# Performance work log

Measured on AMD Instinct MI355X. Metric: run time of the kernel, lower is better.

Reference implementation:

```python
import jax, jax.numpy as jnp
import numpy as np

MAX_DEPTH = 9
HIDDEN = 64
EMB = 64
POS_FREQS = 6
IN_C = 1
SIZES = [4 ** d for d in range(MAX_DEPTH + 1)]
OFFSETS = np.concatenate([[0], np.cumsum(SIZES)])  # per-depth slices into concatenated node arrays
TOTAL = int(OFFSETS[-1])  # 349525
POS_DIM = 3 + 2 * POS_FREQS * 3  # 39


def _interleave(v):
    v = v & 0xFFFF
    v = (v | (v << 8)) & 0x00FF00FF
    v = (v | (v << 4)) & 0x0F0F0F0F
    v = (v | (v << 2)) & 0x33333333
    v = (v | (v << 1)) & 0x55555555
    return v


def _deinterleave(v):
    v = v & 0x55555555
    v = (v | (v >> 1)) & 0x33333333
    v = (v | (v >> 2)) & 0x0F0F0F0F
    v = (v | (v >> 4)) & 0x00FF00FF
    v = (v | (v >> 8)) & 0x0000FFFF
    return v


def _xy(d):
    keys = jnp.arange(4 ** d, dtype=jnp.int32)  # full tree: sorted Morton keys = arange
    return _deinterleave(keys), _deinterleave(keys >> 1)


def _neighbors(d):
    # [N, 9] neighbor indices in Morton order grid; -1 outside the image (matches quadtree.neighs padding)
    ix, iy = _xy(d)
    res = 1 << d
    cols = []
    for dy in (-1, 0, 1):
        for dx in (-1, 0, 1):
            nx, ny = ix + dx, iy + dy
            valid = (nx >= 0) & (nx < res) & (ny >= 0) & (ny < res)
            key = _interleave(nx) | (_interleave(ny) << 1)
            cols.append(jnp.where(valid, key, -1))
    return jnp.stack(cols, axis=1)


def _pos_enc(d):
    # node_centers_from_keys + fourier_encode
    ix, iy = _xy(d)
    res = float(1 << d)
    x = (ix.astype(jnp.float32) + 0.5) / res
    y = (iy.astype(jnp.float32) + 0.5) / res
    dn = jnp.full_like(x, float(d) / float(MAX_DEPTH))
    pos = jnp.stack([x, y, dn], axis=1)  # [N, 3]
    freqs = 2.0 ** jnp.arange(POS_FREQS, dtype=jnp.float32)
    ang = pos[:, :, None] * (2.0 * np.pi) * freqs  # [N, 3, F]
    enc = jnp.concatenate([jnp.sin(ang), jnp.cos(ang)], axis=-1).reshape(pos.shape[0], -1)  # [N, 3*2F]
    return jnp.concatenate([pos, enc], axis=1)  # [N, 39]


def setup_inputs() -> dict:
    key = jax.random.key(0)
    ks = jax.random.split(key, 10)
    s = 0.05
    return {
        "features_in": jax.random.normal(ks[0], (TOTAL, IN_C), jnp.float32),
        "in_proj_W": jax.random.normal(ks[1], (IN_C + POS_DIM, HIDDEN), jnp.float32) * s,
        "in_proj_b": jnp.zeros((HIDDEN,), jnp.float32),
        "conv_W": jax.random.normal(ks[2], (MAX_DEPTH + 1, 9 * HIDDEN, HIDDEN), jnp.float32) * s,
        "conv_b": jnp.zeros((MAX_DEPTH + 1, HIDDEN), jnp.float32),
        "emb_W": jax.random.normal(ks[3], (MAX_DEPTH + 1, HIDDEN, EMB), jnp.float32) * s,
        "emb_b": jnp.zeros((MAX_DEPTH + 1, EMB), jnp.float32),
        "ln_g": jnp.ones((MAX_DEPTH + 1, EMB), jnp.float32),
        "ln_b": jnp.zeros((MAX_DEPTH + 1, EMB), jnp.float32),
        "depth_gain": jnp.ones((MAX_DEPTH + 1,), jnp.float32),
    }


def reference(features_in, in_proj_W, in_proj_b, conv_W, conv_b, emb_W, emb_b, ln_g, ln_b, depth_gain):
    D = MAX_DEPTH
    # per-depth input projection with fourier positional encoding
    h = []
    for d in range(D + 1):
        f = features_in[OFFSETS[d]:OFFSETS[d + 1]]
        x = jnp.concatenate([f, _pos_enc(d)], axis=1)  # [N_d, in_c + 39]
        h.append(x @ in_proj_W + in_proj_b)
    # bottom-up: QuadPool (mean over 4 children; full tree => children of parent i are 4i..4i+3) + QuadConv
    for d in range(D, 0, -1):
        Np = 4 ** (d - 1)
        pooled = h[d].reshape(Np, 4, HIDDEN).mean(axis=1)
        hd1 = h[d - 1] + pooled
        if d - 1 >= 1:
            neigh = _neighbors(d - 1)  # [N, 9], -1 at borders
            N = neigh.shape[0]
            padded = jnp.concatenate([hd1, jnp.zeros((1, HIDDEN), hd1.dtype)], axis=0)
            gi = jnp.where(neigh < 0, N, neigh)
            col = padded[gi].reshape(N, 9 * HIDDEN)
            hd1 = jax.nn.relu(col @ conv_W[d - 1] + conv_b[d - 1])
        h[d - 1] = hd1
    # per-depth embedding head: Linear -> LayerNorm -> depth gain
    outs = []
    eps = 1e-5
    for d in range(D + 1):
        z = h[d] @ emb_W[d] + emb_b[d]
        mu = z.mean(-1, keepdims=True)
        var = ((z - mu) ** 2).mean(-1, keepdims=True)
        z = (z - mu) / jnp.sqrt(var + eps) * ln_g[d] + ln_b[d]
        outs.append(depth_gain[d] * z)
    return jnp.concatenate(outs, axis=0)  # [TOTAL, EMB] (E[0]..E[max_depth] concatenated)
```

## Files before the change

### kernel.cpp

```cpp
#include <hip/hip_runtime.h>
#include <hip/hip_bf16.h>

static constexpr int TOTAL = 349525;
static constexpr int OFFS[11] = {0,1,5,21,85,341,1365,5461,21845,87381,349525};
static constexpr size_t CONV_USH = (size_t)8*9*2*4*64*8;
static constexpr size_t EMB_USH  = (size_t)10*2*4*64*8;
static constexpr size_t FRAG_USH = CONV_USH + EMB_USH;
static constexpr size_t FRAG_BYTES = FRAG_USH*2*2;
static constexpr size_t HPRE_BYTES = (size_t)(87381-85)*64*4;

typedef __attribute__((ext_vector_type(8))) short short8;
typedef __attribute__((ext_vector_type(4))) float f32x4;

__device__ __forceinline__ unsigned deint(unsigned v){
  v &= 0x55555555u;
  v = (v | (v>>1)) & 0x33333333u;
  v = (v | (v>>2)) & 0x0F0F0F0Fu;
  v = (v | (v>>4)) & 0x00FF00FFu;
  v = (v | (v>>8)) & 0x0000FFFFu;
  return v;
}
__device__ __forceinline__ unsigned ileave(unsigned v){
  v &= 0xFFFFu;
  v = (v | (v<<8)) & 0x00FF00FFu;
  v = (v | (v<<4)) & 0x0F0F0F0Fu;
  v = (v | (v<<2)) & 0x33333333u;
  v = (v | (v<<1)) & 0x55555555u;
  return v;
}
__device__ __forceinline__ unsigned short f2bh(float x){
  unsigned u = __float_as_uint(x);
  return (unsigned short)((u + 0x7FFFu + ((u>>16)&1u)) >> 16);
}
__device__ __forceinline__ float bh2f(unsigned short h){
  return __uint_as_float(((unsigned)h) << 16);
}
__device__ __forceinline__ void split8(float4 a, float4 b, short8 &hi, short8 &lo){
  float v[8] = {a.x,a.y,a.z,a.w,b.x,b.y,b.z,b.w};
  unsigned short hv[8], lv[8];
  #pragma unroll
  for (int j=0;j<8;++j){ hv[j]=f2bh(v[j]); lv[j]=f2bh(v[j]-bh2f(hv[j])); }
  hi = short8{(short)hv[0],(short)hv[1],(short)hv[2],(short)hv[3],
              (short)hv[4],(short)hv[5],(short)hv[6],(short)hv[7]};
  lo = short8{(short)lv[0],(short)lv[1],(short)lv[2],(short)lv[3],
              (short)lv[4],(short)lv[5],(short)lv[6],(short)lv[7]};
}

__global__ __launch_bounds__(256) void k_wprep(const float* __restrict__ convW,
    const float* __restrict__ embW,
    unsigned short* __restrict__ WH, unsigned short* __restrict__ WLo){
  int tid = blockIdx.x*256 + threadIdx.x;
  if (tid >= 41984) return;
  const float* src;
  size_t dst;
  if (tid < 36864){
    int l=tid&63, cb=(tid>>6)&3, ks=(tid>>8)&1;
    int x=tid>>9; int m=x%9, Lp=x/9;
    int k0=ks*32+((l>>4)<<3), ch=cb*16+(l&15);
    src = convW + (size_t)(Lp+1)*36864 + (size_t)(m*64+k0)*64 + ch;
    dst = (size_t)tid*8;
  } else {
    int t2 = tid - 36864;
    int l=t2&63, cb=(t2>>6)&3, ks=(t2>>8)&1, d=t2>>9;
    int k0=ks*32+((l>>4)<<3), ch=cb*16+(l&15);
    src = embW + (size_t)d*4096 + (size_t)k0*64 + ch;
    dst = CONV_USH + (size_t)t2*8;
  }
  unsigned short hv[8], lv[8];
  #pragma unroll
  for (int j=0;j<8;++j){
    float v = src[(size_t)j*64];
    unsigned short h = f2bh(v);
    hv[j] = h;
    lv[j] = f2bh(v - bh2f(h));
  }
  short8 vh = {(short)hv[0],(short)hv[1],(short)hv[2],(short)hv[3],
               (short)hv[4],(short)hv[5],(short)hv[6],(short)hv[7]};
  short8 vl = {(short)lv[0],(short)lv[1],(short)lv[2],(short)lv[3],
               (short)lv[4],(short)lv[5],(short)lv[6],(short)lv[7]};
  *(short8*)(WH  + dst) = vh;
  *(short8*)(WLo + dst) = vl;
}

__global__ __launch_bounds__(256) void k_inproj(const float* __restrict__ feat,
    const float* __restrict__ W, const float* __restrict__ B,
    float* __restrict__ h, float* __restrict__ hpre){
  __shared__ float Alt[128][44];
  __shared__ float Wl[40][68];
  int t = threadIdx.x;
  int base = blockIdx.x * 128;
  for (int idx = t; idx < 40*64; idx += 256)
    Wl[idx >> 6][idx & 63] = W[idx];
  if (t < 128){
    int g = base + t;
    float* row = Alt[t];
    if (g < TOTAL){
      int d = 0;
      #pragma unroll
      for (int i = 1; i <= 9; ++i) if (g >= OFFS[i]) d = i;
      int local = g - OFFS[d];
      unsigned ix = deint((unsigned)local), iy = deint(((unsigned)local) >> 1);
      float inv = 1.0f / (float)(1 << d);
      float px = ((float)ix + 0.5f) * inv;
      float py = ((float)iy + 0.5f) * inv;
      float pd = (float)d * (1.0f/9.0f);
      row[0] = feat[g]; row[1] = px; row[2] = py; row[3] = pd;
      float p3[3] = {px, py, pd};
      #pragma unroll
      for (int c = 0; c < 3; ++c){
        float s, co;
        __sincosf(6.28318530717958647692f * p3[c], &s, &co);
        float* rb = row + 4 + c*12;
        #pragma unroll
        for (int f = 0; f < 6; ++f){
          rb[f] = s; rb[6+f] = co;
          float s2 = 2.f*s*co, c2 = 1.f - 2.f*s*s;
          s = s2; co = c2;
        }
      }
    } else {
      #pragma unroll
      for (int k = 0; k < 40; ++k) row[k] = 0.f;
    }
  }
  __syncthreads();
  int tr = t >> 3, tc = t & 7;
  float acc[4][8];
  #pragma unroll
  for (int i=0;i<4;++i)
    #pragma unroll
    for (int c=0;c<8;++c) acc[i][c] = 0.f;
  #pragma unroll 2
  for (int k4 = 0; k4 < 10; ++k4){
    float av4[4][4];
    #pragma unroll
    for (int i=0;i<4;++i){
      float4 aa = *(const float4*)&Alt[tr*4+i][k4*4];
      av4[i][0]=aa.x; av4[i][1]=aa.y; av4[i][2]=aa.z; av4[i][3]=aa.w;
    }
    #pragma unroll
    for (int j=0;j<4;++j){
      float4 lo = *(const float4*)&Wl[k4*4+j][tc*8];
      float4 hi = *(const float4*)&Wl[k4*4+j][tc*8+4];
      float wv[8];
      wv[0]=lo.x; wv[1]=lo.y; wv[2]=lo.z; wv[3]=lo.w;
      wv[4]=hi.x; wv[5]=hi.y; wv[6]=hi.z; wv[7]=hi.w;
      #pragma unroll
      for (int i=0;i<4;++i){
        float a = av4[i][j];
        #pragma unroll
        for (int c=0;c<8;++c) acc[i][c] += a*wv[c];
      }
    }
  }
  #pragma unroll
  for (int i=0;i<4;++i){
    int g = base + tr*4 + i;
    if (g >= TOTAL) continue;
    float ov[8];
    #pragma unroll
    for (int c=0;c<8;++c) ov[c] = acc[i][c] + B[tc*8+c];
    float* dst = &h[(size_t)g*64 + tc*8];
    *(float4*)dst       = *(const float4*)&ov[0];
    *(float4*)(dst + 4) = *(const float4*)&ov[4];
    if (hpre && g >= OFFS[4] && g < OFFS[9]){
      float* dp = hpre + (size_t)(g - OFFS[4])*64 + tc*8;
      *(float4*)dp       = *(const float4*)&ov[0];
      *(float4*)(dp + 4) = *(const float4*)&ov[4];
    }
  }
}

__global__ __launch_bounds__(256) void k_conv(float* __restrict__ h,
    const float* __restrict__ hPar,
    const unsigned short* __restrict__ WHl, const unsigned short* __restrict__ WLl,
    const float* __restrict__ Bb, int N, int offL, int offC, int lbits){
  __shared__ unsigned short haloH[100*72];
  __shared__ unsigned short haloL[100*72];
  __shared__ int hkey[100];
  int t = threadIdx.x;
  int nb = blockIdx.x * 64;
  int res = 1 << lbits;
  if (t < 100){
    int i = t % 10, j = t / 10;
    int gx = (int)deint((unsigned)nb) - 1 + i;
    int gy = (int)deint(((unsigned)nb)>>1) - 1 + j;
    bool ok = (gx>=0 && gy>=0 && gx<res && gy<res);
    hkey[t] = ok ? (int)(ileave((unsigned)gx) | (ileave((unsigned)gy)<<1)) : -1;
  }
  __syncthreads();
  const float* hC = h + (size_t)offC*64;
  for (int e = t; e < 1600; e += 256){
    int hi_ = e >> 4, u = e & 15;
    int key = hkey[hi_];
    float4 r = make_float4(0.f,0.f,0.f,0.f);
    if (key >= 0){
      const float4* c = (const float4*)(hC + (size_t)(4*key)*64) + u;
      float4 c0 = c[0], c1 = c[16], c2 = c[32], c3 = c[48];
      float4 pr = *((const float4*)(hPar + (size_t)key*64) + u);
      r.x = 0.25f*(c0.x+c1.x+c2.x+c3.x) + pr.x;
      r.y = 0.25f*(c0.y+c1.y+c2.y+c3.y) + pr.y;
      r.z = 0.25f*(c0.z+c1.z+c2.z+c3.z) + pr.z;
      r.w = 0.25f*(c0.w+c1.w+c2.w+c3.w) + pr.w;
    }
    unsigned short h0=f2bh(r.x), h1=f2bh(r.y), h2=f2bh(r.z), h3=f2bh(r.w);
    ushort4 rh = make_ushort4(h0,h1,h2,h3);
    ushort4 rl = make_ushort4(f2bh(r.x - bh2f(h0)), f2bh(r.y - bh2f(h1)),
                              f2bh(r.z - bh2f(h2)), f2bh(r.w - bh2f(h3)));
    *(ushort4*)&haloH[hi_*72 + u*4] = rh;
    *(ushort4*)&haloL[hi_*72 + u*4] = rl;
  }
  __syncthreads();

  int cb   = __builtin_amdgcn_readfirstlane((int)(threadIdx.x >> 6));
  int lane = t & 63;
  int q = lane >> 4;
  int chl = cb*16 + (lane & 15);
  int lx0,ly0,lx1,ly1,lx2,ly2,lx3,ly3;
  {
    int n0 = (lane&15), n1 = 16+(lane&15), n2 = 32+(lane&15), n3 = 48+(lane&15);
    lx0=(int)deint((unsigned)n0); ly0=(int)deint(((unsigned)n0)>>1);
    lx1=(int)deint((unsigned)n1); ly1=(int)deint(((unsigned)n1)>>1);
    lx2=(int)deint((unsigned)n2); ly2=(int)deint(((unsigned)n2)>>1);
    lx3=(int)deint((unsigned)n3); ly3=(int)deint(((unsigned)n3)>>1);
  }
  f32x4 acc0 = {0.f,0.f,0.f,0.f}, acc1 = acc0, acc2 = acc0, acc3 = acc0;

  #pragma unroll 1
  for (int dy=0;dy<3;++dy){
    #pragma unroll 1
    for (int dx=0;dx<3;++dx){
      int m = dy*3 + dx;
      int r0 = (ly0+dy)*10 + lx0+dx;
      int r1 = (ly1+dy)*10 + lx1+dx;
      int r2 = (ly2+dy)*10 + lx2+dx;
      int r3 = (ly3+dy)*10 + lx3+dx;
      #pragma unroll
      for (int ks=0;ks<2;++ks){
        const unsigned short* fp = WHl + ((size_t)((m*2+ks)*4 + cb)*64 + lane)*8;
        const unsigned short* fq = WLl + ((size_t)((m*2+ks)*4 + cb)*64 + lane)*8;
        short8 bh = *(const short8*)fp;
        short8 bl = *(const short8*)fq;
        int so = (ks*4 + q)*8;
        short8 ah0 = *(const short8*)&haloH[r0*72 + so];
        short8 al0 = *(const short8*)&haloL[r0*72 + so];
        short8 ah1 = *(const short8*)&haloH[r1*72 + so];
        short8 al1 = *(const short8*)&haloL[r1*72 + so];
        short8 ah2 = *(const short8*)&haloH[r2*72 + so];
        short8 al2 = *(const short8*)&haloL[r2*72 + so];
        short8 ah3 = *(const short8*)&haloH[r3*72 + so];
        short8 al3 = *(const short8*)&haloL[r3*72 + so];
        acc0 = __builtin_amdgcn_mfma_f32_16x16x32_bf16(ah0, bh, acc0, 0,0,0);
        acc1 = __builtin_amdgcn_mfma_f32_16x16x32_bf16(ah1, bh, acc1, 0,0,0);
        acc2 = __builtin_amdgcn_mfma_f32_16x16x32_bf16(ah2, bh, acc2, 0,0,0);
        acc3 = __builtin_amdgcn_mfma_f32_16x16x32_bf16(ah3, bh, acc3, 0,0,0);
        acc0 = __builtin_amdgcn_mfma_f32_16x16x32_bf16(al0, bh, acc0, 0,0,0);
        acc1 = __builtin_amdgcn_mfma_f32_16x16x32_bf16(al1, bh, acc1, 0,0,0);
        acc2 = __builtin_amdgcn_mfma_f32_16x16x32_bf16(al2, bh, acc2, 0,0,0);
        acc3 = __builtin_amdgcn_mfma_f32_16x16x32_bf16(al3, bh, acc3, 0,0,0);
        acc0 = __builtin_amdgcn_mfma_f32_16x16x32_bf16(ah0, bl, acc0, 0,0,0);
        acc1 = __builtin_amdgcn_mfma_f32_16x16x32_bf16(ah1, bl, acc1, 0,0,0);
        acc2 = __builtin_amdgcn_mfma_f32_16x16x32_bf16(ah2, bl, acc2, 0,0,0);
        acc3 = __builtin_amdgcn_mfma_f32_16x16x32_bf16(ah3, bl, acc3, 0,0,0);
      }
    }
  }
  float bias = Bb[chl];
  int rowb = q*4;
  float* hO = h + (size_t)(offL + nb)*64;
  #pragma unroll
  for (int reg=0;reg<4;++reg){
    int n0 = rowb + reg;
    float v0 = acc0[reg] + bias; if (nb + n0      < N) hO[(size_t)(n0     )*64 + chl] = v0 > 0.f ? v0 : 0.f;
    float v1 = acc1[reg] + bias; if (nb + n0 + 16 < N) hO[(size_t)(n0 + 16)*64 + chl] = v1 > 0.f ? v1 : 0.f;
    float v2 = acc2[reg] + bias; if (nb + n0 + 32 < N) hO[(size_t)(n0 + 32)*64 + chl] = v2 > 0.f ? v2 : 0.f;
    float v3 = acc3[reg] + bias; if (nb + n0 + 48 < N) hO[(size_t)(n0 + 48)*64 + chl] = v3 > 0.f ? v3 : 0.f;
  }
}

__device__ __forceinline__ void emb_tile(float* __restrict__ h,
    const unsigned short* __restrict__ EH, const unsigned short* __restrict__ ELo,
    const float* __restrict__ embB, const float* __restrict__ lng,
    const float* __restrict__ lnb, const float* __restrict__ gain,
    int d, size_t rowbase, int validN, int lane){
  int q = lane >> 4, li = lane & 15;
  const float* rp = h + (rowbase + li)*64 + q*8;
  float4 a0 = *(const float4*)rp;
  float4 a1 = *(const float4*)(rp + 4);
  float4 a2 = *(const float4*)(rp + 32);
  float4 a3 = *(const float4*)(rp + 36);
  short8 ah0, al0, ah1, al1;
  split8(a0, a1, ah0, al0);
  split8(a2, a3, ah1, al1);
  f32x4 acc0 = {0.f,0.f,0.f,0.f}, acc1 = acc0, acc2 = acc0, acc3 = acc0;
  #define EMB_CB(CB, ACC) { \
    size_t f0 = (((size_t)(d*2+0)*4 + (CB))*64 + lane)*8; \
    size_t f1 = (((size_t)(d*2+1)*4 + (CB))*64 + lane)*8; \
    short8 bh0 = *(const short8*)(EH + f0); \
    short8 bl0 = *(const short8*)(ELo + f0); \
    short8 bh1 = *(const short8*)(EH + f1); \
    short8 bl1 = *(const short8*)(ELo + f1); \
    ACC = __builtin_amdgcn_mfma_f32_16x16x32_bf16(ah0, bh0, ACC, 0,0,0); \
    ACC = __builtin_amdgcn_mfma_f32_16x16x32_bf16(al0, bh0, ACC, 0,0,0); \
    ACC = __builtin_amdgcn_mfma_f32_16x16x32_bf16(ah0, bl0, ACC, 0,0,0); \
    ACC = __builtin_amdgcn_mfma_f32_16x16x32_bf16(ah1, bh1, ACC, 0,0,0); \
    ACC = __builtin_amdgcn_mfma_f32_16x16x32_bf16(al1, bh1, ACC, 0,0,0); \
    ACC = __builtin_amdgcn_mfma_f32_16x16x32_bf16(ah1, bl1, ACC, 0,0,0); }
  EMB_CB(0, acc0)
  EMB_CB(1, acc1)
  EMB_CB(2, acc2)
  EMB_CB(3, acc3)
  #undef EMB_CB
  float b0 = embB[d*64 +      li];
  float b1 = embB[d*64 + 16 + li];
  float b2 = embB[d*64 + 32 + li];
  float b3 = embB[d*64 + 48 + li];
  float mu[4], rs[4];
  float z0[4], z1[4], z2[4], z3[4];
  #pragma unroll
  for (int r=0;r<4;++r){
    z0[r] = acc0[r] + b0;
    z1[r] = acc1[r] + b1;
    z2[r] = acc2[r] + b2;
    z3[r] = acc3[r] + b3;
    float s  = z0[r] + z1[r] + z2[r] + z3[r];
    float qv = z0[r]*z0[r] + z1[r]*z1[r] + z2[r]*z2[r] + z3[r]*z3[r];
    #pragma unroll
    for (int mk=1; mk<16; mk<<=1){
      s  += __shfl_xor(s, mk, 64);
      qv += __shfl_xor(qv, mk, 64);
    }
    float m = s * 0.015625f;
    mu[r] = m;
    rs[r] = rsqrtf(qv * 0.015625f - m*m + 1e-5f);
  }
  float g0 = lng[d*64 +      li], l0 = lnb[d*64 +      li];
  float g1 = lng[d*64 + 16 + li], l1 = lnb[d*64 + 16 + li];
  float g2 = lng[d*64 + 32 + li], l2 = lnb[d*64 + 32 + li];
  float g3 = lng[d*64 + 48 + li], l3 = lnb[d*64 + 48 + li];
  float gn = gain[d];
  #pragma unroll
  for (int r=0;r<4;++r){
    int ni = q*4 + r;
    if (ni < validN){
      float* row = h + (rowbase + ni)*64;
      row[     li] = ((z0[r] - mu[r])*rs[r]*g0 + l0)*gn;
      row[16 + li] = ((z1[r] - mu[r])*rs[r]*g1 + l1)*gn;
      row[32 + li] = ((z2[r] - mu[r])*rs[r]*g2 + l2)*gn;
      row[48 + li] = ((z3[r] - mu[r])*rs[r]*g3 + l3)*gn;
    }
  }
}

template<int L>
__device__ __forceinline__ void tail_level2(float* __restrict__ h,
    const unsigned short* __restrict__ WHc, const unsigned short* __restrict__ WLc,
    const float* __restrict__ convB, const float* __restrict__ Hpar,
    unsigned short* __restrict__ PtH, unsigned short* __restrict__ PtL, int t){
  constexpr int Np  = 1 << (2*L);
  constexpr int NTt = (Np + 15)/16;
  constexpr int TG  = (NTt + 3)/4;
  constexpr int res = 1 << L;
  int w  = t >> 6;
  int cb = __builtin_amdgcn_readfirstlane(w & 3);
  int tg = __builtin_amdgcn_readfirstlane(w >> 2);
  int lane = t & 63;
  int q = lane >> 4, li = lane & 15;
  int chl = cb*16 + li;
  int lx[TG], ly[TG];
  #pragma unroll
  for (int i=0;i<TG;++i){
    unsigned n = (unsigned)((tg*TG + i)*16 + li);
    lx[i] = (int)deint(n); ly[i] = (int)deint(n >> 1);
  }
  f32x4 acc[TG];
  #pragma unroll
  for (int i=0;i<TG;++i) acc[i] = f32x4{0.f,0.f,0.f,0.f};
  short8 bh0, bl0, bh1, bl1;
  {
    size_t f0 = ((size_t)(0*4 + cb)*64 + lane)*8;
    size_t f1 = ((size_t)(1*4 + cb)*64 + lane)*8;
    bh0 = *(const short8*)(WHc + f0); bl0 = *(const short8*)(WLc + f0);
    bh1 = *(const short8*)(WHc + f1); bl1 = *(const short8*)(WLc + f1);
  }
  #pragma unroll 1
  for (int m=0;m<9;++m){
    short8 nh0, nl0, nh1, nl1;
    if (m < 8){
      size_t f0 = ((size_t)(((m+1)*2+0)*4 + cb)*64 + lane)*8;
      size_t f1 = ((size_t)(((m+1)*2+1)*4 + cb)*64 + lane)*8;
      nh0 = *(const short8*)(WHc + f0); nl0 = *(const short8*)(WLc + f0);
      nh1 = *(const short8*)(WHc + f1); nl1 = *(const short8*)(WLc + f1);
    }
    int dy = m/3 - 1, dx = m%3 - 1;
    #pragma unroll
    for (int i=0;i<TG;++i){
      int nx = lx[i]+dx, ny = ly[i]+dy;
      int key = (nx>=0 && ny>=0 && nx<res && ny<res)
              ? (int)(ileave((unsigned)nx) | (ileave((unsigned)ny)<<1)) : Np;
      const unsigned short* pH = PtH + key*72;
      const unsigned short* pL = PtL + key*72;
      short8 ah0 = *(const short8*)(pH + q*8);
      short8 al0 = *(const short8*)(pL + q*8);
      short8 ah1 = *(const short8*)(pH + 32 + q*8);
      short8 al1 = *(const short8*)(pL + 32 + q*8);
      acc[i] = __builtin_amdgcn_mfma_f32_16x16x32_bf16(ah0, bh0, acc[i], 0,0,0);
      acc[i] = __builtin_amdgcn_mfma_f32_16x16x32_bf16(al0, bh0, acc[i], 0,0,0);
      acc[i] = __builtin_amdgcn_mfma_f32_16x16x32_bf16(ah0, bl0, acc[i], 0,0,0);
      acc[i] = __builtin_amdgcn_mfma_f32_16x16x32_bf16(ah1, bh1, acc[i], 0,0,0);
      acc[i] = __builtin_amdgcn_mfma_f32_16x16x32_bf16(al1, bh1, acc[i], 0,0,0);
      acc[i] = __builtin_amdgcn_mfma_f32_16x16x32_bf16(ah1, bl1, acc[i], 0,0,0);
    }
    if (m < 8){ bh0 = nh0; bl0 = nl0; bh1 = nh1; bl1 = nl1; }
  }
  float bias = convB[L*64 + chl];
  float vq[TG][4];
  #pragma unroll
  for (int i=0;i<TG;++i){
    #pragma unroll
    for (int reg=0;reg<4;++reg){
      int ni = (tg*TG + i)*16 + q*4 + reg;
      float v = acc[i][reg] + bias;
      v = v > 0.f ? v : 0.f;
      vq[i][reg] = v;
      if (ni < Np) h[(size_t)(OFFS[L] + ni)*64 + chl] = v;
    }
  }
  __syncthreads();
  if (L > 1){
    constexpr int Pp = Np/4;
    #pragma unroll
    for (int i=0;i<TG;++i){
      int p = (tg*TG + i)*4 + q;
      if (p < Pp){
        float pooled = 0.25f*(vq[i][0]+vq[i][1]+vq[i][2]+vq[i][3])
                     + Hpar[(size_t)(OFFS[L-1] + p)*64 + chl];
        unsigned short hh = f2bh(pooled);
        PtH[p*72 + chl] = hh;
        PtL[p*72 + chl] = f2bh(pooled - bh2f(hh));
      }
    }
    if (t < 64){ PtH[Pp*72 + t] = 0; PtL[Pp*72 + t] = 0; }
  } else {
    if (tg == 0 && q == 0){
      float pooled = 0.25f*(vq[0][0]+vq[0][1]+vq[0][2]+vq[0][3]) + Hpar[chl];
      h[chl] = pooled;
    }
  }
  __syncthreads();
}

__global__ __launch_bounds__(1024) void k_tail_emb(float* __restrict__ h,
    const unsigned short* __restrict__ WH, const unsigned short* __restrict__ WLo,
    const float* __restrict__ convB,
    const unsigned short* __restrict__ EH, const unsigned short* __restrict__ ELo,
    const float* __restrict__ embB, const float* __restrict__ lng,
    const float* __restrict__ lnb, const float* __restrict__ gain){
  __shared__ unsigned short PtH[257*72];
  __shared__ unsigned short PtL[257*72];
  __shared__ float Hpar[85*64];
  int t = threadIdx.x;
  if (blockIdx.x != 0){
    int bb = blockIdx.x - 1;
    int d, start;
    if      (bb < 8)  { d=6; start=0;   }
    else if (bb < 40) { d=7; start=8;   }
    else if (bb < 168){ d=8; start=40;  }
    else              { d=9; start=168; }
    size_t base = (size_t)OFFS[d] + (size_t)(bb - start)*512;
    int w = t >> 6, lane = t & 63;
    emb_tile(h, EH, ELo, embB, lng, lnb, gain, d, base + (size_t)w*16,      16, lane);
    emb_tile(h, EH, ELo, embB, lng, lnb, gain, d, base + (size_t)(w+16)*16, 16, lane);
    return;
  }
  for (int e = t; e < 85*16; e += 1024)
    ((float4*)Hpar)[e] = ((const float4*)h)[e];
  for (int e = t; e < 257*16; e += 1024){
    int node = e >> 4, u = e & 15;
    float4 r = make_float4(0.f,0.f,0.f,0.f);
    if (node < 256){
      const float4* c = (const float4*)(h + (size_t)(OFFS[5] + 4*node)*64) + u;
      float4 c0 = c[0], c1 = c[16], c2 = c[32], c3 = c[48];
      float4 pr = *((const float4*)(h + (size_t)(OFFS[4] + node)*64) + u);
      r.x = 0.25f*(c0.x+c1.x+c2.x+c3.x) + pr.x;
      r.y = 0.25f*(c0.y+c1.y+c2.y+c3.y) + pr.y;
      r.z = 0.25f*(c0.z+c1.z+c2.z+c3.z) + pr.z;
      r.w = 0.25f*(c0.w+c1.w+c2.w+c3.w) + pr.w;
    }
    unsigned short h0=f2bh(r.x), h1=f2bh(r.y), h2=f2bh(r.z), h3=f2bh(r.w);
    *(ushort4*)&PtH[node*72 + u*4] = make_ushort4(h0,h1,h2,h3);
    *(ushort4*)&PtL[node*72 + u*4] = make_ushort4(
        f2bh(r.x - bh2f(h0)), f2bh(r.y - bh2f(h1)),
        f2bh(r.z - bh2f(h2)), f2bh(r.w - bh2f(h3)));
  }
  __syncthreads();
  tail_level2<4>(h, WH + (size_t)3*36864, WLo + (size_t)3*36864, convB, Hpar, PtH, PtL, t);
  tail_level2<3>(h, WH + (size_t)2*36864, WLo + (size_t)2*36864, convB, Hpar, PtH, PtL, t);
  tail_level2<2>(h, WH + (size_t)1*36864, WLo + (size_t)1*36864, convB, Hpar, PtH, PtL, t);
  tail_level2<1>(h, WH,                   WLo,                   convB, Hpar, PtH, PtL, t);
  int w = t >> 6, lane = t & 63;
  for (int j = w; j < 87; j += 16){
    int d, tile;
    if (j < 64)      { d=5; tile=j;    }
    else if (j < 80) { d=4; tile=j-64; }
    else if (j < 84) { d=3; tile=j-80; }
    else if (j == 84){ d=2; tile=0;    }
    else if (j == 85){ d=1; tile=0;    }
    else             { d=0; tile=0;    }
    int Nlev = 1 << (2*d);
    emb_tile(h, EH, ELo, embB, lng, lnb, gain, d,
             (size_t)OFFS[d] + (size_t)tile*16, Nlev - tile*16, lane);
  }
}

extern "C" void kernel_launch(void* const* d_in, const int* in_sizes, int n_in,
                              void* d_out, int out_size, void* d_ws, size_t ws_size,
                              hipStream_t stream) {
  (void)in_sizes; (void)n_in; (void)out_size;
  const float* feat  = (const float*)d_in[0];
  const float* ipW   = (const float*)d_in[1];
  const float* ipB   = (const float*)d_in[2];
  const float* convW = (const float*)d_in[3];
  const float* convB = (const float*)d_in[4];
  const float* embW  = (const float*)d_in[5];
  const float* embB  = (const float*)d_in[6];
  const float* lng   = (const float*)d_in[7];
  const float* lnb   = (const float*)d_in[8];
  const float* gain  = (const float*)d_in[9];
  float* h = (float*)d_out;

  unsigned short* WH  = (unsigned short*)d_ws;
  unsigned short* WLo = WH + FRAG_USH;
  float* hpre = (ws_size >= FRAG_BYTES + HPRE_BYTES)
              ? (float*)((char*)d_ws + FRAG_BYTES) : nullptr;

  k_wprep<<<164, 256, 0, stream>>>(convW, embW, WH, WLo);
  k_inproj<<<(TOTAL + 127)/128, 256, 0, stream>>>(feat, ipW, ipB, h, hpre);

  for (int L = 8; L >= 5; --L){
    int Np = 1 << (2*L);
    const float* hPar = hpre ? (hpre + (size_t)(OFFS[L] - OFFS[4])*64)
                             : (h + (size_t)OFFS[L]*64);
    k_conv<<<Np/64, 256, 0, stream>>>(h, hPar,
        WH  + (size_t)(L-1)*36864, WLo + (size_t)(L-1)*36864,
        convB + (size_t)L*64, Np, OFFS[L], OFFS[L+1], L);
  }

  k_tail_emb<<<681, 1024, 0, stream>>>(h, WH, WLo, convB,
      WH + CONV_USH, WLo + CONV_USH, embB, lng, lnb, gain);
}
```

Before: 205.8 us.

## Overlap deep-level embedding heads with conv launches and shrink tail kernel

The conv kernel gains extra blocks that compute the embedding/LayerNorm head for level L+2 while level L is convolved, so levels 6–9 are embedded alongside the under-filled small conv launches. The depth-4 conv moves from the single serial tail block into a multi-block conv launch. The tail kernel now handles only levels 3..1 serially plus embeddings of levels 0–5, with much smaller LDS staging. This removes a long serial critical path in the tail and fills idle CUs during small conv grids, at the cost of an extra launch and larger conv grids.

```diff
diff --git a/kernel.cpp b/kernel.cpp
--- a/kernel.cpp
+++ b/kernel.cpp
@@ -171,113 +171,6 @@
   }
 }
 
-__global__ __launch_bounds__(256) void k_conv(float* __restrict__ h,
-    const float* __restrict__ hPar,
-    const unsigned short* __restrict__ WHl, const unsigned short* __restrict__ WLl,
-    const float* __restrict__ Bb, int N, int offL, int offC, int lbits){
-  __shared__ unsigned short haloH[100*72];
-  __shared__ unsigned short haloL[100*72];
-  __shared__ int hkey[100];
-  int t = threadIdx.x;
-  int nb = blockIdx.x * 64;
-  int res = 1 << lbits;
-  if (t < 100){
-    int i = t % 10, j = t / 10;
-    int gx = (int)deint((unsigned)nb) - 1 + i;
-    int gy = (int)deint(((unsigned)nb)>>1) - 1 + j;
-    bool ok = (gx>=0 && gy>=0 && gx<res && gy<res);
-    hkey[t] = ok ? (int)(ileave((unsigned)gx) | (ileave((unsigned)gy)<<1)) : -1;
-  }
-  __syncthreads();
-  const float* hC = h + (size_t)offC*64;
-  for (int e = t; e < 1600; e += 256){
-    int hi_ = e >> 4, u = e & 15;
-    int key = hkey[hi_];
-    float4 r = make_float4(0.f,0.f,0.f,0.f);
-    if (key >= 0){
-      const float4* c = (const float4*)(hC + (size_t)(4*key)*64) + u;
-      float4 c0 = c[0], c1 = c[16], c2 = c[32], c3 = c[48];
-      float4 pr = *((const float4*)(hPar + (size_t)key*64) + u);
-      r.x = 0.25f*(c0.x+c1.x+c2.x+c3.x) + pr.x;
-      r.y = 0.25f*(c0.y+c1.y+c2.y+c3.y) + pr.y;
-      r.z = 0.25f*(c0.z+c1.z+c2.z+c3.z) + pr.z;
-      r.w = 0.25f*(c0.w+c1.w+c2.w+c3.w) + pr.w;
-    }
-    unsigned short h0=f2bh(r.x), h1=f2bh(r.y), h2=f2bh(r.z), h3=f2bh(r.w);
-    ushort4 rh = make_ushort4(h0,h1,h2,h3);
-    ushort4 rl = make_ushort4(f2bh(r.x - bh2f(h0)), f2bh(r.y - bh2f(h1)),
-                              f2bh(r.z - bh2f(h2)), f2bh(r.w - bh2f(h3)));
-    *(ushort4*)&haloH[hi_*72 + u*4] = rh;
-    *(ushort4*)&haloL[hi_*72 + u*4] = rl;
-  }
-  __syncthreads();
-
-  int cb   = __builtin_amdgcn_readfirstlane((int)(threadIdx.x >> 6));
-  int lane = t & 63;
-  int q = lane >> 4;
-  int chl = cb*16 + (lane & 15);
-  int lx0,ly0,lx1,ly1,lx2,ly2,lx3,ly3;
-  {
-    int n0 = (lane&15), n1 = 16+(lane&15), n2 = 32+(lane&15), n3 = 48+(lane&15);
-    lx0=(int)deint((unsigned)n0); ly0=(int)deint(((unsigned)n0)>>1);
-    lx1=(int)deint((unsigned)n1); ly1=(int)deint(((unsigned)n1)>>1);
-    lx2=(int)deint((unsigned)n2); ly2=(int)deint(((unsigned)n2)>>1);
-    lx3=(int)deint((unsigned)n3); ly3=(int)deint(((unsigned)n3)>>1);
-  }
-  f32x4 acc0 = {0.f,0.f,0.f,0.f}, acc1 = acc0, acc2 = acc0, acc3 = acc0;
-
-  #pragma unroll 1
-  for (int dy=0;dy<3;++dy){
-    #pragma unroll 1
-    for (int dx=0;dx<3;++dx){
-      int m = dy*3 + dx;
-      int r0 = (ly0+dy)*10 + lx0+dx;
-      int r1 = (ly1+dy)*10 + lx1+dx;
-      int r2 = (ly2+dy)*10 + lx2+dx;
-      int r3 = (ly3+dy)*10 + lx3+dx;
-      #pragma unroll
-      for (int ks=0;ks<2;++ks){
-        const unsigned short* fp = WHl + ((size_t)((m*2+ks)*4 + cb)*64 + lane)*8;
-        const unsigned short* fq = WLl + ((size_t)((m*2+ks)*4 + cb)*64 + lane)*8;
-        short8 bh = *(const short8*)fp;
-        short8 bl = *(const short8*)fq;
-        int so = (ks*4 + q)*8;
-        short8 ah0 = *(const short8*)&haloH[r0*72 + so];
-        short8 al0 = *(const short8*)&haloL[r0*72 + so];
-        short8 ah1 = *(const short8*)&haloH[r1*72 + so];
-        short8 al1 = *(const short8*)&haloL[r1*72 + so];
-        short8 ah2 = *(const short8*)&haloH[r2*72 + so];
-        short8 al2 = *(const short8*)&haloL[r2*72 + so];
-        short8 ah3 = *(const short8*)&haloH[r3*72 + so];
-        short8 al3 = *(const short8*)&haloL[r3*72 + so];
-        acc0 = __builtin_amdgcn_mfma_f32_16x16x32_bf16(ah0, bh, acc0, 0,0,0);
-        acc1 = __builtin_amdgcn_mfma_f32_16x16x32_bf16(ah1, bh, acc1, 0,0,0);
-        acc2 = __builtin_amdgcn_mfma_f32_16x16x32_bf16(ah2, bh, acc2, 0,0,0);
-        acc3 = __builtin_amdgcn_mfma_f32_16x16x32_bf16(ah3, bh, acc3, 0,0,0);
-        acc0 = __builtin_amdgcn_mfma_f32_16x16x32_bf16(al0, bh, acc0, 0,0,0);
-        acc1 = __builtin_amdgcn_mfma_f32_16x16x32_bf16(al1, bh, acc1, 0,0,0);
-        acc2 = __builtin_amdgcn_mfma_f32_16x16x32_bf16(al2, bh, acc2, 0,0,0);
-        acc3 = __builtin_amdgcn_mfma_f32_16x16x32_bf16(al3, bh, acc3, 0,0,0);
-        acc0 = __builtin_amdgcn_mfma_f32_16x16x32_bf16(ah0, bl, acc0, 0,0,0);
-        acc1 = __builtin_amdgcn_mfma_f32_16x16x32_bf16(ah1, bl, acc1, 0,0,0);
-        acc2 = __builtin_amdgcn_mfma_f32_16x16x32_bf16(ah2, bl, acc2, 0,0,0);
-        acc3 = __builtin_amdgcn_mfma_f32_16x16x32_bf16(ah3, bl, acc3, 0,0,0);
-      }
-    }
-  }
-  float bias = Bb[chl];
-  int rowb = q*4;
-  float* hO = h + (size_t)(offL + nb)*64;
-  #pragma unroll
-  for (int reg=0;reg<4;++reg){
-    int n0 = rowb + reg;
-    float v0 = acc0[reg] + bias; if (nb + n0      < N) hO[(size_t)(n0     )*64 + chl] = v0 > 0.f ? v0 : 0.f;
-    float v1 = acc1[reg] + bias; if (nb + n0 + 16 < N) hO[(size_t)(n0 + 16)*64 + chl] = v1 > 0.f ? v1 : 0.f;
-    float v2 = acc2[reg] + bias; if (nb + n0 + 32 < N) hO[(size_t)(n0 + 32)*64 + chl] = v2 > 0.f ? v2 : 0.f;
-    float v3 = acc3[reg] + bias; if (nb + n0 + 48 < N) hO[(size_t)(n0 + 48)*64 + chl] = v3 > 0.f ? v3 : 0.f;
-  }
-}
-
 __device__ __forceinline__ void emb_tile(float* __restrict__ h,
     const unsigned short* __restrict__ EH, const unsigned short* __restrict__ ELo,
     const float* __restrict__ embB, const float* __restrict__ lng,
@@ -352,6 +245,122 @@
   }
 }
 
+__global__ __launch_bounds__(256) void k_conv_emb(float* __restrict__ h,
+    const float* __restrict__ hPar,
+    const unsigned short* __restrict__ WHl, const unsigned short* __restrict__ WLl,
+    const float* __restrict__ Bb, int N, int offL, int offC, int lbits, int NC,
+    const unsigned short* __restrict__ EH, const unsigned short* __restrict__ ELo,
+    const float* __restrict__ embB, const float* __restrict__ lng,
+    const float* __restrict__ lnb, const float* __restrict__ gain, int embD){
+  __shared__ unsigned short haloH[100*72];
+  __shared__ unsigned short haloL[100*72];
+  __shared__ int hkey[100];
+  int t = threadIdx.x;
+  if ((int)blockIdx.x >= NC){
+    int b2 = blockIdx.x - NC;
+    int w = t >> 6, lane = t & 63;
+    size_t base = (size_t)OFFS[embD] + ((size_t)b2*4 + w)*16;
+    emb_tile(h, EH, ELo, embB, lng, lnb, gain, embD, base, 16, lane);
+    return;
+  }
+  int nb = blockIdx.x * 64;
+  int res = 1 << lbits;
+  if (t < 100){
+    int i = t % 10, j = t / 10;
+    int gx = (int)deint((unsigned)nb) - 1 + i;
+    int gy = (int)deint(((unsigned)nb)>>1) - 1 + j;
+    bool ok = (gx>=0 && gy>=0 && gx<res && gy<res);
+    hkey[t] = ok ? (int)(ileave((unsigned)gx) | (ileave((unsigned)gy)<<1)) : -1;
+  }
+  __syncthreads();
+  const float* hC = h + (size_t)offC*64;
+  for (int e = t; e < 1600; e += 256){
+    int hi_ = e >> 4, u = e & 15;
+    int key = hkey[hi_];
+    float4 r = make_float4(0.f,0.f,0.f,0.f);
+    if (key >= 0){
+      const float4* c = (const float4*)(hC + (size_t)(4*key)*64) + u;
+      float4 c0 = c[0], c1 = c[16], c2 = c[32], c3 = c[48];
+      float4 pr = *((const float4*)(hPar + (size_t)key*64) + u);
+      r.x = 0.25f*(c0.x+c1.x+c2.x+c3.x) + pr.x;
+      r.y = 0.25f*(c0.y+c1.y+c2.y+c3.y) + pr.y;
+      r.z = 0.25f*(c0.z+c1.z+c2.z+c3.z) + pr.z;
+      r.w = 0.25f*(c0.w+c1.w+c2.w+c3.w) + pr.w;
+    }
+    unsigned short h0=f2bh(r.x), h1=f2bh(r.y), h2=f2bh(r.z), h3=f2bh(r.w);
+    *(ushort4*)&haloH[hi_*72 + u*4] = make_ushort4(h0,h1,h2,h3);
+    *(ushort4*)&haloL[hi_*72 + u*4] = make_ushort4(
+        f2bh(r.x - bh2f(h0)), f2bh(r.y - bh2f(h1)),
+        f2bh(r.z - bh2f(h2)), f2bh(r.w - bh2f(h3)));
+  }
+  __syncthreads();
+
+  int cb   = __builtin_amdgcn_readfirstlane((int)(threadIdx.x >> 6));
+  int lane = t & 63;
+  int q = lane >> 4;
+  int chl = cb*16 + (lane & 15);
+  int lx0,ly0,lx1,ly1,lx2,ly2,lx3,ly3;
+  {
+    int n0 = (lane&15), n1 = 16+(lane&15), n2 = 32+(lane&15), n3 = 48+(lane&15);
+    lx0=(int)deint((unsigned)n0); ly0=(int)deint(((unsigned)n0)>>1);
+    lx1=(int)deint((unsigned)n1); ly1=(int)deint(((unsigned)n1)>>1);
+    lx2=(int)deint((unsigned)n2); ly2=(int)deint(((unsigned)n2)>>1);
+    lx3=(int)deint((unsigned)n3); ly3=(int)deint(((unsigned)n3)>>1);
+  }
+  f32x4 acc0 = {0.f,0.f,0.f,0.f}, acc1 = acc0, acc2 = acc0, acc3 = acc0;
+
+  #pragma unroll 1
+  for (int dy=0;dy<3;++dy){
+    #pragma unroll 1
+    for (int dx=0;dx<3;++dx){
+      int m = dy*3 + dx;
+      int r0 = (ly0+dy)*10 + lx0+dx;
+      int r1 = (ly1+dy)*10 + lx1+dx;
+      int r2 = (ly2+dy)*10 + lx2+dx;
+      int r3 = (ly3+dy)*10 + lx3+dx;
+      #pragma unroll
+      for (int ks=0;ks<2;++ks){
+        const unsigned short* fp = WHl + ((size_t)((m*2+ks)*4 + cb)*64 + lane)*8;
+        const unsigned short* fq = WLl + ((size_t)((m*2+ks)*4 + cb)*64 + lane)*8;
+        short8 bh = *(const short8*)fp;
+        short8 bl = *(const short8*)fq;
+        int so = (ks*4 + q)*8;
+        short8 ah0 = *(const short8*)&haloH[r0*72 + so];
+        short8 al0 = *(const short8*)&haloL[r0*72 + so];
+        short8 ah1 = *(const short8*)&haloH[r1*72 + so];
+        short8 al1 = *(const short8*)&haloL[r1*72 + so];
+        short8 ah2 = *(const short8*)&haloH[r2*72 + so];
+        short8 al2 = *(const short8*)&haloL[r2*72 + so];
+        short8 ah3 = *(const short8*)&haloH[r3*72 + so];
+        short8 al3 = *(const short8*)&haloL[r3*72 + so];
+        acc0 = __builtin_amdgcn_mfma_f32_16x16x32_bf16(ah0, bh, acc0, 0,0,0);
+        acc1 = __builtin_amdgcn_mfma_f32_16x16x32_bf16(ah1, bh, acc1, 0,0,0);
+        acc2 = __builtin_amdgcn_mfma_f32_16x16x32_bf16(ah2, bh, acc2, 0,0,0);
+        acc3 = __builtin_amdgcn_mfma_f32_16x16x32_bf16(ah3, bh, acc3, 0,0,0);
+        acc0 = __builtin_amdgcn_mfma_f32_16x16x32_bf16(al0, bh, acc0, 0,0,0);
+        acc1 = __builtin_amdgcn_mfma_f32_16x16x32_bf16(al1, bh, acc1, 0,0,0);
+        acc2 = __builtin_amdgcn_mfma_f32_16x16x32_bf16(al2, bh, acc2, 0,0,0);
+        acc3 = __builtin_amdgcn_mfma_f32_16x16x32_bf16(al3, bh, acc3, 0,0,0);
+        acc0 = __builtin_amdgcn_mfma_f32_16x16x32_bf16(ah0, bl, acc0, 0,0,0);
+        acc1 = __builtin_amdgcn_mfma_f32_16x16x32_bf16(ah1, bl, acc1, 0,0,0);
+        acc2 = __builtin_amdgcn_mfma_f32_16x16x32_bf16(ah2, bl, acc2, 0,0,0);
+        acc3 = __builtin_amdgcn_mfma_f32_16x16x32_bf16(ah3, bl, acc3, 0,0,0);
+      }
+    }
+  }
+  float bias = Bb[chl];
+  int rowb = q*4;
+  float* hO = h + (size_t)(offL + nb)*64;
+  #pragma unroll
+  for (int reg=0;reg<4;++reg){
+    int n0 = rowb + reg;
+    float v0 = acc0[reg] + bias; if (nb + n0      < N) hO[(size_t)(n0     )*64 + chl] = v0 > 0.f ? v0 : 0.f;
+    float v1 = acc1[reg] + bias; if (nb + n0 + 16 < N) hO[(size_t)(n0 + 16)*64 + chl] = v1 > 0.f ? v1 : 0.f;
+    float v2 = acc2[reg] + bias; if (nb + n0 + 32 < N) hO[(size_t)(n0 + 32)*64 + chl] = v2 > 0.f ? v2 : 0.f;
+    float v3 = acc3[reg] + bias; if (nb + n0 + 48 < N) hO[(size_t)(n0 + 48)*64 + chl] = v3 > 0.f ? v3 : 0.f;
+  }
+}
+
 template<int L>
 __device__ __forceinline__ void tail_level2(float* __restrict__ h,
     const unsigned short* __restrict__ WHc, const unsigned short* __restrict__ WLc,
@@ -450,38 +459,31 @@
   __syncthreads();
 }
 
-__global__ __launch_bounds__(1024) void k_tail_emb(float* __restrict__ h,
+__global__ __launch_bounds__(1024) void k_tail(float* __restrict__ h,
     const unsigned short* __restrict__ WH, const unsigned short* __restrict__ WLo,
     const float* __restrict__ convB,
     const unsigned short* __restrict__ EH, const unsigned short* __restrict__ ELo,
     const float* __restrict__ embB, const float* __restrict__ lng,
     const float* __restrict__ lnb, const float* __restrict__ gain){
-  __shared__ unsigned short PtH[257*72];
-  __shared__ unsigned short PtL[257*72];
+  __shared__ unsigned short PtH[65*72];
+  __shared__ unsigned short PtL[65*72];
   __shared__ float Hpar[85*64];
   int t = threadIdx.x;
+  int w = t >> 6, lane = t & 63;
   if (blockIdx.x != 0){
-    int bb = blockIdx.x - 1;
-    int d, start;
-    if      (bb < 8)  { d=6; start=0;   }
-    else if (bb < 40) { d=7; start=8;   }
-    else if (bb < 168){ d=8; start=40;  }
-    else              { d=9; start=168; }
-    size_t base = (size_t)OFFS[d] + (size_t)(bb - start)*512;
-    int w = t >> 6, lane = t & 63;
-    emb_tile(h, EH, ELo, embB, lng, lnb, gain, d, base + (size_t)w*16,      16, lane);
-    emb_tile(h, EH, ELo, embB, lng, lnb, gain, d, base + (size_t)(w+16)*16, 16, lane);
+    size_t base = (size_t)OFFS[5] + ((size_t)(blockIdx.x - 1)*16 + w)*16;
+    emb_tile(h, EH, ELo, embB, lng, lnb, gain, 5, base, 16, lane);
     return;
   }
   for (int e = t; e < 85*16; e += 1024)
     ((float4*)Hpar)[e] = ((const float4*)h)[e];
-  for (int e = t; e < 257*16; e += 1024){
+  for (int e = t; e < 65*16; e += 1024){
     int node = e >> 4, u = e & 15;
     float4 r = make_float4(0.f,0.f,0.f,0.f);
-    if (node < 256){
-      const float4* c = (const float4*)(h + (size_t)(OFFS[5] + 4*node)*64) + u;
+    if (node < 64){
+      const float4* c = (const float4*)(h + (size_t)(OFFS[4] + 4*node)*64) + u;
       float4 c0 = c[0], c1 = c[16], c2 = c[32], c3 = c[48];
-      float4 pr = *((const float4*)(h + (size_t)(OFFS[4] + node)*64) + u);
+      float4 pr = *((const float4*)(h + (size_t)(OFFS[3] + node)*64) + u);
       r.x = 0.25f*(c0.x+c1.x+c2.x+c3.x) + pr.x;
       r.y = 0.25f*(c0.y+c1.y+c2.y+c3.y) + pr.y;
       r.z = 0.25f*(c0.z+c1.z+c2.z+c3.z) + pr.z;
@@ -494,22 +496,20 @@
         f2bh(r.z - bh2f(h2)), f2bh(r.w - bh2f(h3)));
   }
   __syncthreads();
-  tail_level2<4>(h, WH + (size_t)3*36864, WLo + (size_t)3*36864, convB, Hpar, PtH, PtL, t);
   tail_level2<3>(h, WH + (size_t)2*36864, WLo + (size_t)2*36864, convB, Hpar, PtH, PtL, t);
   tail_level2<2>(h, WH + (size_t)1*36864, WLo + (size_t)1*36864, convB, Hpar, PtH, PtL, t);
   tail_level2<1>(h, WH,                   WLo,                   convB, Hpar, PtH, PtL, t);
-  int w = t >> 6, lane = t & 63;
-  for (int j = w; j < 87; j += 16){
+  for (int j = w; j < 23; j += 16){
     int d, tile;
-    if (j < 64)      { d=5; tile=j;    }
-    else if (j < 80) { d=4; tile=j-64; }
-    else if (j < 84) { d=3; tile=j-80; }
-    else if (j == 84){ d=2; tile=0;    }
-    else if (j == 85){ d=1; tile=0;    }
+    if (j < 16)      { d=4; tile=j;    }
+    else if (j < 20) { d=3; tile=j-16; }
+    else if (j == 20){ d=2; tile=0;    }
+    else if (j == 21){ d=1; tile=0;    }
     else             { d=0; tile=0;    }
     int Nlev = 1 << (2*d);
+    int valid = Nlev - tile*16;
     emb_tile(h, EH, ELo, embB, lng, lnb, gain, d,
-             (size_t)OFFS[d] + (size_t)tile*16, Nlev - tile*16, lane);
+             (size_t)OFFS[d] + (size_t)tile*16, valid > 16 ? 16 : valid, lane);
   }
 }
 
@@ -531,21 +531,27 @@
 
   unsigned short* WH  = (unsigned short*)d_ws;
   unsigned short* WLo = WH + FRAG_USH;
+  const unsigned short* EH  = WH  + CONV_USH;
+  const unsigned short* ELo = WLo + CONV_USH;
   float* hpre = (ws_size >= FRAG_BYTES + HPRE_BYTES)
               ? (float*)((char*)d_ws + FRAG_BYTES) : nullptr;
 
   k_wprep<<<164, 256, 0, stream>>>(convW, embW, WH, WLo);
   k_inproj<<<(TOTAL + 127)/128, 256, 0, stream>>>(feat, ipW, ipB, h, hpre);
 
-  for (int L = 8; L >= 5; --L){
+  for (int L = 8; L >= 4; --L){
     int Np = 1 << (2*L);
+    int NC = Np/64;
+    int embD = (L <= 7) ? L + 2 : -1;
+    int embBlocks = (embD > 0) ? (1 << (2*embD)) / 64 : 0;
     const float* hPar = hpre ? (hpre + (size_t)(OFFS[L] - OFFS[4])*64)
                              : (h + (size_t)OFFS[L]*64);
-    k_conv<<<Np/64, 256, 0, stream>>>(h, hPar,
+    k_conv_emb<<<NC + embBlocks, 256, 0, stream>>>(h, hPar,
         WH  + (size_t)(L-1)*36864, WLo + (size_t)(L-1)*36864,
-        convB + (size_t)L*64, Np, OFFS[L], OFFS[L+1], L);
-  }
-
-  k_tail_emb<<<681, 1024, 0, stream>>>(h, WH, WLo, convB,
-      WH + CONV_USH, WLo + CONV_USH, embB, lng, lnb, gain);
-}
+        convB + (size_t)L*64, Np, OFFS[L], OFFS[L+1], L, NC,
+        EH, ELo, embB, lng, lnb, gain, embD);
+  }
+
+  k_tail<<<5, 1024, 0, stream>>>(h, WH, WLo, convB,
+      EH, ELo, embB, lng, lnb, gain);
+}
```

Result: faster. 200.0 us (-2.8%).
